# Performance work log

Measured on AMD Instinct MI355X. Metric: run time of the kernel, lower is better.

The kernel has to match this reference:

```python
import jax, jax.numpy as jnp
import numpy as np

N = 5000        # nodes
F = 7699        # node feature dim (fixed by code)
E = 40000       # edges
ED = 3          # edge_dim (fixed by code)
H1, C1 = 4, 1024
H2, C2 = 1, 1024
NUM_OUT = 128
NEG_SLOPE = 0.2


def _glorot(key, shape):
    fan_in = shape[0]
    return jax.random.normal(key, shape, jnp.float32) / np.float32(np.sqrt(fan_in))


def setup_inputs() -> dict:
    key = jax.random.key(0)
    ks = jax.random.split(key, 16)
    x = jax.random.normal(ks[0], (N, F), jnp.float32)
    src = jax.random.randint(ks[1], (E,), 0, N)
    dst = jax.random.randint(ks[2], (E,), 0, N)
    src = jnp.where(src == dst, (src + 1) % N, src)  # no pre-existing self loops
    edge_index = jnp.stack([src, dst]).astype(jnp.int32)
    edge_attr = jax.random.normal(ks[3], (E, ED), jnp.float32)
    inp = {
        "x": x, "edge_index": edge_index, "edge_attr": edge_attr,
        # GATv2Conv #1: 7699 -> 1024, heads=4, edge_dim=3
        "W1l": _glorot(ks[4], (F, H1 * C1)), "b1l": jnp.zeros((H1 * C1,), jnp.float32),
        "W1r": _glorot(ks[5], (F, H1 * C1)), "b1r": jnp.zeros((H1 * C1,), jnp.float32),
        "W1e": _glorot(ks[6], (ED, H1 * C1)),
        "att1": _glorot(ks[7], (H1, C1)),
        "bias1": jnp.zeros((H1 * C1,), jnp.float32),
        # GATv2Conv #2: 4096 -> 1024, heads=1, edge_dim=3
        "W2l": _glorot(ks[8], (H1 * C1, H2 * C2)), "b2l": jnp.zeros((H2 * C2,), jnp.float32),
        "W2r": _glorot(ks[9], (H1 * C1, H2 * C2)), "b2r": jnp.zeros((H2 * C2,), jnp.float32),
        "W2e": _glorot(ks[10], (ED, H2 * C2)),
        "att2": _glorot(ks[11], (H2, C2)),
        "bias2": jnp.zeros((H2 * C2,), jnp.float32),
        # final Linear(1024, num_outputs)
        "Wlin": _glorot(ks[12], (C2, NUM_OUT)), "blin": jnp.zeros((NUM_OUT,), jnp.float32),
    }
    return inp


def gatv2_layer(x, src, dst, edge_attr, Wl, bl, Wr, br, We, att, bias, heads, out_ch):
    """PyG GATv2Conv with add_self_loops=True, fill_value='mean', concat=True."""
    n = x.shape[0]
    # self-loop edge_attr = mean of incoming edge attrs per node (fill_value='mean')
    deg = jax.ops.segment_sum(jnp.ones((src.shape[0],), jnp.float32), dst, num_segments=n)
    loop_attr = jax.ops.segment_sum(edge_attr, dst, num_segments=n) / jnp.maximum(deg, 1.0)[:, None]
    idx = jnp.arange(n, dtype=src.dtype)
    srcf = jnp.concatenate([src, idx])
    dstf = jnp.concatenate([dst, idx])
    ea = jnp.concatenate([edge_attr, loop_attr], axis=0)
    xl = (x @ Wl + bl).reshape(n, heads, out_ch)   # lin_l (source)
    xr = (x @ Wr + br).reshape(n, heads, out_ch)   # lin_r (target)
    ee = (ea @ We).reshape(-1, heads, out_ch)       # lin_edge (no bias)
    e = jax.nn.leaky_relu(xl[srcf] + xr[dstf] + ee, NEG_SLOPE)  # [E', H, C]
    logit = jnp.einsum('ehc,hc->eh', e, att)                     # [E', H]
    # segment softmax over destination nodes (every node has a self loop)
    m = jax.lax.stop_gradient(jax.ops.segment_max(logit, dstf, num_segments=n))
    a = jnp.exp(logit - m[dstf])
    denom = jax.ops.segment_sum(a, dstf, num_segments=n)
    alpha = a / (denom[dstf] + 1e-16)
    out = jax.ops.segment_sum(alpha[:, :, None] * xl[srcf], dstf, num_segments=n)  # [N,H,C]
    return out.reshape(n, heads * out_ch) + bias


def reference(x, edge_index, edge_attr,
              W1l, b1l, W1r, b1r, W1e, att1, bias1,
              W2l, b2l, W2r, b2r, W2e, att2, bias2,
              Wlin, blin):
    src, dst = edge_index[0], edge_index[1]
    h = gatv2_layer(x, src, dst, edge_attr, W1l, b1l, W1r, b1r, W1e, att1, bias1, H1, C1)
    h = gatv2_layer(h, src, dst, edge_attr, W2l, b2l, W2r, b2r, W2e, att2, bias2, H2, C2)
    return h @ Wlin + blin
```

## Files before the change

kernel.cpp:

```cpp
#include <hip/hip_runtime.h>
#include <cstdint>
#include <cstddef>

#define N_NODES 5000
#define F_IN    7699
#define KP1     7712
#define KT1     241
#define MP      5120
#define E_EDGES 40000
#define EFULL   45000
#define HC1     4096
#define N1      8192
#define HC2     1024
#define N2      2048
#define NOUT    128
#define GM      (MP / 256)

typedef __bf16 bf16x8 __attribute__((ext_vector_type(8)));
typedef float  f32x4  __attribute__((ext_vector_type(4)));
typedef float  f32x16 __attribute__((ext_vector_type(16)));
typedef unsigned short u16x8 __attribute__((ext_vector_type(8)));
typedef _Float16 f16;
typedef _Float16 f16x8 __attribute__((ext_vector_type(8)));

using as1_uchar = unsigned char __attribute__((address_space(1)));
using as3_uchar = unsigned char __attribute__((address_space(3)));

__device__ __forceinline__ unsigned short f2bf(float f) {
  union { float f; unsigned int u; } v; v.f = f;
  return (unsigned short)((v.u + 0x7fffu + ((v.u >> 16) & 1u)) >> 16);
}
__device__ __forceinline__ float bf2f(unsigned short h) {
  union { unsigned int u; float f; } v; v.u = ((unsigned int)h) << 16;
  return v.f;
}

__device__ __forceinline__ void gload16(const void* g, void* l) {
  __builtin_amdgcn_global_load_lds(
      reinterpret_cast<const as1_uchar*>(reinterpret_cast<uintptr_t>(g)),
      reinterpret_cast<as3_uchar*>(reinterpret_cast<uintptr_t>(l)),
      16, 0, 0);
}



__global__ void k_split_x(const float* __restrict__ x, unsigned short* __restrict__ hi,
                          unsigned short* __restrict__ lo) {
  const int C8 = KP1 / 8;
  int ci = blockIdx.x * 256 + threadIdx.x;
  if (ci >= MP * C8) return;
  int r = ci / C8, c8 = ci % C8;
  int c = c8 * 8;
  u16x8 hb, lb;
  #pragma unroll
  for (int j = 0; j < 8; ++j) {
    float v = 0.f;
    if (r < N_NODES && (c + j) < F_IN) v = x[(size_t)r * F_IN + c + j];
    unsigned short h = f2bf(v);
    hb[j] = h; lb[j] = f2bf(v - bf2f(h));
  }
  size_t off = ((size_t)((r >> 7) * KT1 + (c >> 5)) * 4 + ((c >> 3) & 3)) * 1024 + (r & 127) * 8;
  *(u16x8*)&hi[off] = hb;
  *(u16x8*)&lo[off] = lb;
}


__global__ void k_split_w(const float* __restrict__ W,
                          unsigned short* __restrict__ hi, unsigned short* __restrict__ lo,
                          int K, int Nsrc, int c0, int KT, int rowOffset) {
  __shared__ float tile[32][33];
  const int tid = threadIdx.x;
  const int kt = blockIdx.x;
  const int n0 = blockIdx.y * 32;
  #pragma unroll
  for (int i = tid >> 5; i < 32; i += 8) {
    int k = kt * 32 + i;
    tile[i][tid & 31] = (k < K) ? W[(size_t)k * Nsrc + c0 + n0 + (tid & 31)] : 0.f;
  }
  __syncthreads();
  if (tid < 128) {
    const int nn = tid >> 2, kc = (tid & 3) << 3;
    const int n = rowOffset + n0 + nn;
    u16x8 hb, lb;
    #pragma unroll
    for (int j = 0; j < 8; ++j) {
      float v = tile[kc + j][nn];
      unsigned short h = f2bf(v);
      hb[j] = h; lb[j] = f2bf(v - bf2f(h));
    }
    size_t off = ((size_t)((n >> 7) * KT + kt) * 4 + (kc >> 3)) * 1024 + (n & 127) * 8;
    *(u16x8*)&hi[off] = hb;
    *(u16x8*)&lo[off] = lb;
  }
}


template <int OF16>
__global__ __launch_bounds__(256, 1) void k_gemm_bb(
    const unsigned short* __restrict__ Ahi, const unsigned short* __restrict__ Alo,
    const unsigned short* __restrict__ Bhi, const unsigned short* __restrict__ Blo,
    void* __restrict__ Cp, const float* __restrict__ bias0, const float* __restrict__ bias1,
    int halfN, int M, int Nc, int ldC, int KT32, int nbn)
{
  __shared__ __align__(16) unsigned short S[3 * 16384];

  const int tid = threadIdx.x;
  const int lane = tid & 63;
  const int w = tid >> 6;
  const int wm = w >> 1, wn = w & 1;

  const int nwg = gridDim.x;
  const int qq = nwg >> 3, rr = nwg & 7;
  const int xcd = blockIdx.x & 7, idx = blockIdx.x >> 3;
  const int wg = (xcd < rr ? xcd * (qq + 1) : rr * (qq + 1) + (xcd - rr) * qq) + idx;
  const int bm = wg / nbn, bn = wg % nbn;

  f32x16 acc[4][4] = {};

  const unsigned short* gbase = (w == 0) ? Ahi : (w == 1) ? Alo : (w == 2) ? Bhi : Blo;
  const int brow = (w < 2) ? bm * 2 : bn * 2;
  const unsigned short* gsrc[8];
  int dd[8];
  #pragma unroll
  for (int d = 0; d < 8; ++d) {
    const int t = d >> 2, p = (d >> 1) & 1, hf = d & 1;
    gsrc[d] = gbase + (size_t)(brow + t) * KT32 * 4096 + p * 1024 + hf * 512 + lane * 8;
    dd[d] = w * 4096 + t * 2048 + p * 1024 + hf * 512;
  }

  auto stage = [&](int kt16, int bufo) {
    const size_t o = (size_t)kt16 * 2048;
    #pragma unroll
    for (int d = 0; d < 8; ++d) gload16(gsrc[d] + o, &S[bufo + dd[d]]);
  };

  const int r5 = lane & 31, h5 = lane >> 5;
  int ra[4], cb[4];
  #pragma unroll
  for (int i = 0; i < 4; ++i) ra[i] = wm * 2048 + h5 * 1024 + (i * 32 + r5) * 8;
  #pragma unroll
  for (int j = 0; j < 4; ++j) cb[j] = 8192 + wn * 2048 + h5 * 1024 + (j * 32 + r5) * 8;

  const int KT16 = KT32 * 2;

  stage(0, 0);
  stage(1, 16384);
  asm volatile("s_waitcnt vmcnt(8)" ::: "memory");
  __builtin_amdgcn_s_barrier();

  int ocur = 0, onxt = 16384, onx2 = 32768;
  for (int kt = 0; kt < KT16; ++kt) {
    const int ks = (kt + 2 < KT16) ? kt + 2 : KT16 - 1;
    stage(ks, onx2);

    bf16x8 ah[4], al[4], bh[4], bl[4];
    #pragma unroll
    for (int i = 0; i < 4; ++i) {
      ah[i] = *(const bf16x8*)&S[ocur + ra[i]];
      al[i] = *(const bf16x8*)&S[ocur + 4096 + ra[i]];
    }
    #pragma unroll
    for (int j = 0; j < 4; ++j) {
      bh[j] = *(const bf16x8*)&S[ocur + cb[j]];
      bl[j] = *(const bf16x8*)&S[ocur + 4096 + cb[j]];
    }

    __builtin_amdgcn_s_setprio(1);
    #pragma unroll
    for (int j = 0; j < 4; ++j)
      #pragma unroll
      for (int i = 0; i < 4; ++i) {
        acc[i][j] = __builtin_amdgcn_mfma_f32_32x32x16_bf16(ah[i], bh[j], acc[i][j], 0, 0, 0);
        acc[i][j] = __builtin_amdgcn_mfma_f32_32x32x16_bf16(al[i], bh[j], acc[i][j], 0, 0, 0);
        acc[i][j] = __builtin_amdgcn_mfma_f32_32x32x16_bf16(ah[i], bl[j], acc[i][j], 0, 0, 0);
      }
    __builtin_amdgcn_s_setprio(0);

    asm volatile("s_waitcnt vmcnt(8)" ::: "memory");
    __builtin_amdgcn_s_barrier();
    const int t = ocur; ocur = onxt; onxt = onx2; onx2 = t;
  }

  #pragma unroll
  for (int i = 0; i < 4; ++i) {
    #pragma unroll
    for (int j = 0; j < 4; ++j) {
      const int gc = bn * 256 + wn * 128 + j * 32 + r5;
      if (gc < Nc) {
        const float bv = (gc < halfN) ? bias0[gc] : bias1[gc - halfN];
        #pragma unroll
        for (int reg = 0; reg < 16; ++reg) {
          const int gr = bm * 256 + wm * 128 + i * 32 + (reg & 3) + 8 * (reg >> 2) + 4 * h5;
          if (gr < M) {
            float v = acc[i][j][reg] + bv;
            if (OF16) ((f16*)Cp)[(size_t)gr * ldC + gc] = (f16)v;
            else      ((float*)Cp)[(size_t)gr * ldC + gc] = v;
          }
        }
      }
    }
  }
}


__global__ void k_deg(const int* __restrict__ dst, const float* __restrict__ ea,
                      float* __restrict__ deg, float* __restrict__ lattr, int E) {
  int e = blockIdx.x * 256 + threadIdx.x;
  if (e >= E) return;
  int d = dst[e];
  atomicAdd(&deg[d], 1.f);
  atomicAdd(&lattr[d * 3 + 0], ea[e * 3 + 0]);
  atomicAdd(&lattr[d * 3 + 1], ea[e * 3 + 1]);
  atomicAdd(&lattr[d * 3 + 2], ea[e * 3 + 2]);
}

__global__ void k_lattr_fin(float* __restrict__ lattr, const float* __restrict__ deg, int n) {
  int i = blockIdx.x * 256 + threadIdx.x;
  if (i >= n) return;
  float dv = fmaxf(deg[i], 1.f);
  lattr[i * 3 + 0] /= dv; lattr[i * 3 + 1] /= dv; lattr[i * 3 + 2] /= dv;
}

__global__ void k_eafull(const float* __restrict__ ea, const float* __restrict__ lattr,
                         float* __restrict__ eaf, int E, int n) {
  int e = blockIdx.x * 256 + threadIdx.x;
  if (e >= E + n) return;
  const float* s = (e < E) ? &ea[(size_t)e * 3] : &lattr[(size_t)(e - E) * 3];
  eaf[e * 3 + 0] = s[0]; eaf[e * 3 + 1] = s[1]; eaf[e * 3 + 2] = s[2];
}

__global__ void k_count(const int* __restrict__ dst, int* __restrict__ cnt, int E, int n) {
  int e = blockIdx.x * 256 + threadIdx.x;
  if (e >= E + n) return;
  int d = (e < E) ? dst[e] : (e - E);
  atomicAdd(&cnt[d], 1);
}

__global__ void k_scan(const int* __restrict__ cnt, int* __restrict__ rowptr, int n) {
  int lane = threadIdx.x;
  int run = 0;
  for (int base = 0; base < n; base += 64) {
    int i = base + lane;
    int v = (i < n) ? cnt[i] : 0;
    #pragma unroll
    for (int off = 1; off < 64; off <<= 1) {
      int t = __shfl_up(v, off, 64);
      if (lane >= off) v += t;
    }
    if (i < n) rowptr[i + 1] = run + v;
    run += __shfl(v, 63, 64);
  }
  if (lane == 0) rowptr[0] = 0;
}

__global__ void k_fill(const int* __restrict__ dst, const int* __restrict__ rowptr,
                       int* __restrict__ fillc, int* __restrict__ elist, int E, int n) {
  int e = blockIdx.x * 256 + threadIdx.x;
  if (e >= E + n) return;
  int d = (e < E) ? dst[e] : (e - E);
  int pos = rowptr[d] + atomicAdd(&fillc[d], 1);
  elist[pos] = e;
}


template <int H, int ITERS>
__global__ __launch_bounds__(256) void k_logit(
    const f16* __restrict__ xl, const f16* __restrict__ xr, int strideX,
    const float* __restrict__ eaf, const float* __restrict__ We, const float* __restrict__ att,
    const int* __restrict__ src, const int* __restrict__ dst, int E,
    float* __restrict__ logit)
{
  const int e = blockIdx.x;
  const int tid = threadIdx.x;
  int s, d;
  if (e < E) { s = src[e]; d = dst[e]; } else { s = e - E; d = s; }
  const float ea0 = eaf[e * 3 + 0], ea1 = eaf[e * 3 + 1], ea2 = eaf[e * 3 + 2];
  constexpr int HC = ITERS * 256;
  const f16* rl = xl + (size_t)s * strideX;
  const f16* rr = xr + (size_t)d * strideX;
  float acc[H];
  #pragma unroll
  for (int h = 0; h < H; ++h) acc[h] = 0.f;
  #pragma unroll
  for (int i = 0; i < ITERS; ++i) {
    int hc = tid + (i << 8);
    float v = (float)rl[hc] + (float)rr[hc]
            + ea0 * We[hc] + ea1 * We[HC + hc] + ea2 * We[2 * HC + hc];
    v = (v > 0.f) ? v : 0.2f * v;
    acc[i >> 2] += v * att[hc];
  }
  __shared__ float red[H][4];
  const int lane = tid & 63, wv = tid >> 6;
  #pragma unroll
  for (int h = 0; h < H; ++h) {
    float v = acc[h];
    #pragma unroll
    for (int off = 32; off > 0; off >>= 1) v += __shfl_down(v, off, 64);
    if (lane == 0) red[h][wv] = v;
  }
  __syncthreads();
  if (tid < H)
    logit[(size_t)e * H + tid] = red[tid][0] + red[tid][1] + red[tid][2] + red[tid][3];
}

template <int H>
__global__ void k_stats(const float* __restrict__ logit, const int* __restrict__ rowptr,
                        const int* __restrict__ elist, float* __restrict__ mb, float* __restrict__ db)
{
  const int n = blockIdx.x;
  const int lane = threadIdx.x;
  const int start = rowptr[n], end = rowptr[n + 1];
  #pragma unroll
  for (int h = 0; h < H; ++h) {
    float m = -1e30f;
    for (int p = start + lane; p < end; p += 64)
      m = fmaxf(m, logit[(size_t)elist[p] * H + h]);
    #pragma unroll
    for (int off = 32; off > 0; off >>= 1) m = fmaxf(m, __shfl_down(m, off, 64));
    m = __shfl(m, 0, 64);
    float sum = 0.f;
    for (int p = start + lane; p < end; p += 64)
      sum += __expf(logit[(size_t)elist[p] * H + h] - m);
    #pragma unroll
    for (int off = 32; off > 0; off >>= 1) sum += __shfl_down(sum, off, 64);
    if (lane == 0) { mb[n * H + h] = m; db[n * H + h] = sum; }
  }
}

template <int H, int NC8, int KTo>
__global__ __launch_bounds__(256) void k_agg(
    const f16* __restrict__ xl, int strideX,
    const int* __restrict__ rowptr, const int* __restrict__ elist, const int* __restrict__ src,
    const float* __restrict__ logit, const float* __restrict__ mb, const float* __restrict__ db,
    const float* __restrict__ bias,
    unsigned short* __restrict__ ohi, unsigned short* __restrict__ olo, int E)
{
  const int n = blockIdx.x;
  const int tid = threadIdx.x;
  constexpr int HC = H * 1024;
  float acc[NC8][8];
  #pragma unroll
  for (int q = 0; q < NC8; ++q)
    #pragma unroll
    for (int j = 0; j < 8; ++j) acc[q][j] = 0.f;
  const int start = rowptr[n], end = rowptr[n + 1];
  float mloc[H], dloc[H];
  #pragma unroll
  for (int h = 0; h < H; ++h) { mloc[h] = mb[n * H + h]; dloc[h] = db[n * H + h] + 1e-16f; }
  for (int p = start; p < end; ++p) {
    const int e = elist[p];
    const int s = (e < E) ? src[e] : (e - E);
    float al[H];
    #pragma unroll
    for (int h = 0; h < H; ++h)
      al[h] = __expf(logit[(size_t)e * H + h] - mloc[h]) / dloc[h];
    const f16* row = xl + (size_t)s * strideX;
    #pragma unroll
    for (int q = 0; q < NC8; ++q) {
      const int c8 = tid + q * 256;
      if (c8 * 8 < HC) {
        float a = (H == 4) ? ((tid & 128) ? al[2 * q + 1] : al[2 * q]) : al[0];
        f16x8 v = *(const f16x8*)(row + c8 * 8);
        #pragma unroll
        for (int j = 0; j < 8; ++j) acc[q][j] += a * (float)v[j];
      }
    }
  }
  #pragma unroll
  for (int q = 0; q < NC8; ++q) {
    const int c8 = tid + q * 256;
    if (c8 * 8 < HC) {
      u16x8 hb, lb;
      #pragma unroll
      for (int j = 0; j < 8; ++j) {
        float v = acc[q][j] + bias[c8 * 8 + j];
        unsigned short h = f2bf(v);
        hb[j] = h; lb[j] = f2bf(v - bf2f(h));
      }
      size_t off = ((size_t)((n >> 7) * KTo + (c8 >> 2)) * 4 + (c8 & 3)) * 1024 + (n & 127) * 8;
      *(u16x8*)&ohi[off] = hb;
      *(u16x8*)&olo[off] = lb;
    }
  }
}


extern "C" void kernel_launch(void* const* d_in, const int* in_sizes, int n_in,
                              void* d_out, int out_size, void* d_ws, size_t ws_size,
                              hipStream_t stream) {
  const float* x    = (const float*)d_in[0];
  const int*   eidx = (const int*)d_in[1];
  const float* eattr= (const float*)d_in[2];
  const float* W1l  = (const float*)d_in[3];
  const float* b1l  = (const float*)d_in[4];
  const float* W1r  = (const float*)d_in[5];
  const float* b1r  = (const float*)d_in[6];
  const float* W1e  = (const float*)d_in[7];
  const float* att1 = (const float*)d_in[8];
  const float* bias1= (const float*)d_in[9];
  const float* W2l  = (const float*)d_in[10];
  const float* b2l  = (const float*)d_in[11];
  const float* W2r  = (const float*)d_in[12];
  const float* b2r  = (const float*)d_in[13];
  const float* W2e  = (const float*)d_in[14];
  const float* att2 = (const float*)d_in[15];
  const float* bias2= (const float*)d_in[16];
  const float* Wlin = (const float*)d_in[17];
  const float* blin = (const float*)d_in[18];
  float* out = (float*)d_out;

  char* ws = (char*)d_ws;
  const int* srcp = eidx;
  const int* dstp = eidx + E_EDGES;

  auto alignup = [](size_t v) { return (v + 255) & ~(size_t)255; };

  size_t mo = 0;
  auto take = [&](size_t sz) { size_t r = mo; mo = alignup(mo + sz); return r; };
  const size_t oLATTR = take((size_t)N_NODES * 3 * 4);
  const size_t oDEG   = take((size_t)N_NODES * 4);
  const size_t oEAF   = take((size_t)EFULL * 3 * 4);
  const size_t oCNT   = take((size_t)N_NODES * 4);
  const size_t oROW   = take((size_t)(N_NODES + 1) * 4);
  const size_t oFILL  = take((size_t)N_NODES * 4);
  const size_t oELIST = take((size_t)EFULL * 4);
  const size_t oLOGIT = take((size_t)EFULL * 4 * 4);
  const size_t oMB    = take((size_t)N_NODES * 4 * 4);
  const size_t oDB    = take((size_t)N_NODES * 4 * 4);
  const size_t oXHI   = take((size_t)MP * KP1 * 2);
  const size_t oXLO   = take((size_t)MP * KP1 * 2);
  const size_t oXLR   = take((size_t)N_NODES * N1 * 2);
  const size_t oBH    = take((size_t)N1 * KP1 * 2);
  const size_t oBL    = take((size_t)N1 * KP1 * 2);
  if (ws_size < mo) return;

  const size_t oH1HI = oXHI;
  const size_t oH1LO = oXLO;
  const size_t oXLR2 = oXLR;
  const size_t oH2HI = oXLR + 32ull * 1024 * 1024;
  const size_t oH2LO = oXLR + 48ull * 1024 * 1024;
  const size_t oB2H  = oBH;
  const size_t oB2L  = oBH + 32ull * 1024 * 1024;
  const size_t oB3H  = oBH;
  const size_t oB3L  = oBH + 1ull * 1024 * 1024;

  unsigned short* XHI  = (unsigned short*)(ws + oXHI);
  unsigned short* XLO  = (unsigned short*)(ws + oXLO);
  f16*            XLR  = (f16*)(ws + oXLR);
  unsigned short* BH   = (unsigned short*)(ws + oBH);
  unsigned short* BL   = (unsigned short*)(ws + oBL);
  float*          LATTR= (float*)(ws + oLATTR);
  float*          DEG  = (float*)(ws + oDEG);
  float*          EAF  = (float*)(ws + oEAF);
  int*            CNT  = (int*)(ws + oCNT);
  int*            ROWP = (int*)(ws + oROW);
  int*            FILLC= (int*)(ws + oFILL);
  int*            ELIST= (int*)(ws + oELIST);
  float*          LOGIT= (float*)(ws + oLOGIT);
  float*          MB   = (float*)(ws + oMB);
  float*          DB   = (float*)(ws + oDB);
  unsigned short* H1HI = (unsigned short*)(ws + oH1HI);
  unsigned short* H1LO = (unsigned short*)(ws + oH1LO);
  f16*            XLR2 = (f16*)(ws + oXLR2);
  unsigned short* H2HI = (unsigned short*)(ws + oH2HI);
  unsigned short* H2LO = (unsigned short*)(ws + oH2LO);
  unsigned short* B2H  = (unsigned short*)(ws + oB2H);
  unsigned short* B2L  = (unsigned short*)(ws + oB2L);
  unsigned short* B3H  = (unsigned short*)(ws + oB3H);
  unsigned short* B3L  = (unsigned short*)(ws + oB3L);

  hipMemsetAsync(ws + oDEG,   0, (size_t)N_NODES * 4, stream);
  hipMemsetAsync(ws + oLATTR, 0, (size_t)N_NODES * 3 * 4, stream);
  hipMemsetAsync(ws + oCNT,   0, (size_t)N_NODES * 4, stream);
  hipMemsetAsync(ws + oFILL,  0, (size_t)N_NODES * 4, stream);

  const int gE  = (E_EDGES + 255) / 256;
  const int gEF = (EFULL + 255) / 256;
  const int gN  = (N_NODES + 255) / 256;

  k_deg<<<gE, 256, 0, stream>>>(dstp, eattr, DEG, LATTR, E_EDGES);
  k_lattr_fin<<<gN, 256, 0, stream>>>(LATTR, DEG, N_NODES);
  k_eafull<<<gEF, 256, 0, stream>>>(eattr, LATTR, EAF, E_EDGES, N_NODES);
  k_count<<<gEF, 256, 0, stream>>>(dstp, CNT, E_EDGES, N_NODES);
  k_scan<<<1, 64, 0, stream>>>(CNT, ROWP, N_NODES);
  k_fill<<<gEF, 256, 0, stream>>>(dstp, ROWP, FILLC, ELIST, E_EDGES, N_NODES);

  k_split_x<<<MP * (KP1 / 8) / 256, 256, 0, stream>>>(x, XHI, XLO);
  k_split_w<<<dim3(KT1, HC1 / 32), 256, 0, stream>>>(W1l, BH, BL, F_IN, HC1, 0, KT1, 0);
  k_split_w<<<dim3(KT1, HC1 / 32), 256, 0, stream>>>(W1r, BH, BL, F_IN, HC1, 0, KT1, HC1);
  k_gemm_bb<1><<<GM * (N1 / 256), 256, 0, stream>>>(
      XHI, XLO, BH, BL, XLR, b1l, b1r, HC1, N_NODES, N1, N1, KT1, N1 / 256);

  k_logit<4, 16><<<EFULL, 256, 0, stream>>>(XLR, XLR + HC1, N1, EAF, W1e, att1, srcp, dstp, E_EDGES, LOGIT);
  k_stats<4><<<N_NODES, 64, 0, stream>>>(LOGIT, ROWP, ELIST, MB, DB);
  hipMemsetAsync(ws + oH1HI, 0, (size_t)MP * HC1 * 2, stream);
  hipMemsetAsync(ws + oH1LO, 0, (size_t)MP * HC1 * 2, stream);
  k_agg<4, 2, HC1 / 32><<<N_NODES, 256, 0, stream>>>(
      XLR, N1, ROWP, ELIST, srcp, LOGIT, MB, DB, bias1, H1HI, H1LO, E_EDGES);

  k_split_w<<<dim3(HC1 / 32, HC2 / 32), 256, 0, stream>>>(W2l, B2H, B2L, HC1, HC2, 0, HC1 / 32, 0);
  k_split_w<<<dim3(HC1 / 32, HC2 / 32), 256, 0, stream>>>(W2r, B2H, B2L, HC1, HC2, 0, HC1 / 32, HC2);
  k_gemm_bb<1><<<GM * (N2 / 256), 256, 0, stream>>>(
      H1HI, H1LO, B2H, B2L, XLR2, b2l, b2r, HC2, N_NODES, N2, N2, HC1 / 32, N2 / 256);

  k_logit<1, 4><<<EFULL, 256, 0, stream>>>(XLR2, XLR2 + HC2, N2, EAF, W2e, att2, srcp, dstp, E_EDGES, LOGIT);
  k_stats<1><<<N_NODES, 64, 0, stream>>>(LOGIT, ROWP, ELIST, MB, DB);
  hipMemsetAsync(ws + oH2HI, 0, (size_t)MP * HC2 * 2, stream);
  hipMemsetAsync(ws + oH2LO, 0, (size_t)MP * HC2 * 2, stream);
  k_agg<1, 1, HC2 / 32><<<N_NODES, 256, 0, stream>>>(
      XLR2, N2, ROWP, ELIST, srcp, LOGIT, MB, DB, bias2, H2HI, H2LO, E_EDGES);

  hipMemsetAsync(ws + oB3H, 0, (size_t)2 * 32 * 4096 * 2, stream);
  hipMemsetAsync(ws + oB3L, 0, (size_t)2 * 32 * 4096 * 2, stream);
  k_split_w<<<dim3(HC2 / 32, NOUT / 32), 256, 0, stream>>>(Wlin, B3H, B3L, HC2, NOUT, 0, HC2 / 32, 0);
  k_gemm_bb<0><<<GM * 1, 256, 0, stream>>>(
      H2HI, H2LO, B3H, B3L, out, blin, blin, NOUT, N_NODES, NOUT, NOUT, HC2 / 32, 1);
}
```

Before: 3.003 ms.

## Retile split-bf16 GEMM to 256x128 with 8 waves and 4-stage LDS ring

The GEMM now uses a 256x128 output tile with 512 threads (8 waves, each computing 64x64), instead of a 256x256 tile with 4 waves. The LDS pipeline becomes a four-buffer ring that prefetches three K-steps ahead. The loop is unrolled by two and double-buffers register fragments, so LDS reads for the next step overlap the MFMAs of the current one. The aim is higher occupancy and better latency hiding. In exchange, B-tile reuse per block drops, global traffic for A rises, and the loop assumes an even number of K-steps.

```diff
diff --git a/kernel.cpp b/kernel.cpp
--- a/kernel.cpp
+++ b/kernel.cpp
@@ -96,13 +96,13 @@
 
 
 template <int OF16>
-__global__ __launch_bounds__(256, 1) void k_gemm_bb(
+__global__ __launch_bounds__(512, 2) void k_gemm_bb(
     const unsigned short* __restrict__ Ahi, const unsigned short* __restrict__ Alo,
     const unsigned short* __restrict__ Bhi, const unsigned short* __restrict__ Blo,
     void* __restrict__ Cp, const float* __restrict__ bias0, const float* __restrict__ bias1,
     int halfN, int M, int Nc, int ldC, int KT32, int nbn)
 {
-  __shared__ __align__(16) unsigned short S[3 * 16384];
+  __shared__ __align__(16) unsigned short S[4 * 12288];
 
   const int tid = threadIdx.x;
   const int lane = tid & 63;
@@ -115,82 +115,103 @@
   const int wg = (xcd < rr ? xcd * (qq + 1) : rr * (qq + 1) + (xcd - rr) * qq) + idx;
   const int bm = wg / nbn, bn = wg % nbn;
 
-  f32x16 acc[4][4] = {};
-
-  const unsigned short* gbase = (w == 0) ? Ahi : (w == 1) ? Alo : (w == 2) ? Bhi : Blo;
-  const int brow = (w < 2) ? bm * 2 : bn * 2;
-  const unsigned short* gsrc[8];
-  int dd[8];
-  #pragma unroll
-  for (int d = 0; d < 8; ++d) {
-    const int t = d >> 2, p = (d >> 1) & 1, hf = d & 1;
-    gsrc[d] = gbase + (size_t)(brow + t) * KT32 * 4096 + p * 1024 + hf * 512 + lane * 8;
-    dd[d] = w * 4096 + t * 2048 + p * 1024 + hf * 512;
+  f32x16 acc[2][2] = {};
+
+  const unsigned short* gsrc[3];
+  int dd[3];
+  #pragma unroll
+  for (int s = 0; s < 3; ++s) {
+    const int q = w * 3 + s;
+    const unsigned short* base; int dOff; size_t rowoff; int p, hf;
+    if (q < 8)       { int r_ = q;      base = Ahi; int t = r_ >> 2; p = (r_ >> 1) & 1; hf = r_ & 1;
+                       dOff = t * 2048 + p * 1024 + hf * 512; rowoff = (size_t)(bm * 2 + t) * KT32 * 4096; }
+    else if (q < 16) { int r_ = q - 8;  base = Alo; int t = r_ >> 2; p = (r_ >> 1) & 1; hf = r_ & 1;
+                       dOff = 4096 + t * 2048 + p * 1024 + hf * 512; rowoff = (size_t)(bm * 2 + t) * KT32 * 4096; }
+    else if (q < 20) { int r_ = q - 16; base = Bhi; p = (r_ >> 1) & 1; hf = r_ & 1;
+                       dOff = 8192 + p * 1024 + hf * 512; rowoff = (size_t)bn * KT32 * 4096; }
+    else             { int r_ = q - 20; base = Blo; p = (r_ >> 1) & 1; hf = r_ & 1;
+                       dOff = 10240 + p * 1024 + hf * 512; rowoff = (size_t)bn * KT32 * 4096; }
+    gsrc[s] = base + rowoff + p * 1024 + hf * 512 + lane * 8;
+    dd[s] = dOff;
   }
 
   auto stage = [&](int kt16, int bufo) {
     const size_t o = (size_t)kt16 * 2048;
     #pragma unroll
-    for (int d = 0; d < 8; ++d) gload16(gsrc[d] + o, &S[bufo + dd[d]]);
+    for (int s = 0; s < 3; ++s) gload16(gsrc[s] + o, &S[bufo + dd[s]]);
   };
 
   const int r5 = lane & 31, h5 = lane >> 5;
-  int ra[4], cb[4];
-  #pragma unroll
-  for (int i = 0; i < 4; ++i) ra[i] = wm * 2048 + h5 * 1024 + (i * 32 + r5) * 8;
-  #pragma unroll
-  for (int j = 0; j < 4; ++j) cb[j] = 8192 + wn * 2048 + h5 * 1024 + (j * 32 + r5) * 8;
-
-  const int KT16 = KT32 * 2;
-
-  stage(0, 0);
-  stage(1, 16384);
-  asm volatile("s_waitcnt vmcnt(8)" ::: "memory");
-  __builtin_amdgcn_s_barrier();
-
-  int ocur = 0, onxt = 16384, onx2 = 32768;
-  for (int kt = 0; kt < KT16; ++kt) {
-    const int ks = (kt + 2 < KT16) ? kt + 2 : KT16 - 1;
-    stage(ks, onx2);
-
-    bf16x8 ah[4], al[4], bh[4], bl[4];
-    #pragma unroll
-    for (int i = 0; i < 4; ++i) {
-      ah[i] = *(const bf16x8*)&S[ocur + ra[i]];
-      al[i] = *(const bf16x8*)&S[ocur + 4096 + ra[i]];
-    }
-    #pragma unroll
-    for (int j = 0; j < 4; ++j) {
-      bh[j] = *(const bf16x8*)&S[ocur + cb[j]];
-      bl[j] = *(const bf16x8*)&S[ocur + 4096 + cb[j]];
-    }
-
+  const int tA = wm >> 1;
+  const int rrA = (wm & 1) * 64;
+  int ra[2], cb[2];
+  #pragma unroll
+  for (int i = 0; i < 2; ++i) ra[i] = tA * 2048 + h5 * 1024 + (rrA + i * 32 + r5) * 8;
+  #pragma unroll
+  for (int j = 0; j < 2; ++j) cb[j] = 8192 + h5 * 1024 + (wn * 64 + j * 32 + r5) * 8;
+
+  struct Frags { bf16x8 ah[2], al[2], bh[2], bl[2]; };
+  auto rdfr = [&](Frags& f, int bufo) {
+    #pragma unroll
+    for (int i = 0; i < 2; ++i) {
+      f.ah[i] = *(const bf16x8*)&S[bufo + ra[i]];
+      f.al[i] = *(const bf16x8*)&S[bufo + 4096 + ra[i]];
+    }
+    #pragma unroll
+    for (int j = 0; j < 2; ++j) {
+      f.bh[j] = *(const bf16x8*)&S[bufo + cb[j]];
+      f.bl[j] = *(const bf16x8*)&S[bufo + 2048 + cb[j]];
+    }
+  };
+  auto domfma = [&](Frags& f) {
     __builtin_amdgcn_s_setprio(1);
     #pragma unroll
-    for (int j = 0; j < 4; ++j)
+    for (int j = 0; j < 2; ++j)
       #pragma unroll
-      for (int i = 0; i < 4; ++i) {
-        acc[i][j] = __builtin_amdgcn_mfma_f32_32x32x16_bf16(ah[i], bh[j], acc[i][j], 0, 0, 0);
-        acc[i][j] = __builtin_amdgcn_mfma_f32_32x32x16_bf16(al[i], bh[j], acc[i][j], 0, 0, 0);
-        acc[i][j] = __builtin_amdgcn_mfma_f32_32x32x16_bf16(ah[i], bl[j], acc[i][j], 0, 0, 0);
+      for (int i = 0; i < 2; ++i) {
+        acc[i][j] = __builtin_amdgcn_mfma_f32_32x32x16_bf16(f.ah[i], f.bh[j], acc[i][j], 0, 0, 0);
+        acc[i][j] = __builtin_amdgcn_mfma_f32_32x32x16_bf16(f.al[i], f.bh[j], acc[i][j], 0, 0, 0);
+        acc[i][j] = __builtin_amdgcn_mfma_f32_32x32x16_bf16(f.ah[i], f.bl[j], acc[i][j], 0, 0, 0);
       }
     __builtin_amdgcn_s_setprio(0);
-
-    asm volatile("s_waitcnt vmcnt(8)" ::: "memory");
+  };
+
+  const int KT16 = KT32 * 2;
+
+  stage(0, 0);
+  stage(1, 12288);
+  stage(2, 24576);
+  asm volatile("s_waitcnt vmcnt(3)" ::: "memory");
+  __builtin_amdgcn_s_barrier();
+  Frags fA, fB;
+  rdfr(fA, 0);
+
+  int o0 = 0, o1 = 12288, o2 = 24576, o3 = 36864;
+  for (int kt = 0; kt < KT16; kt += 2) {
+    stage((kt + 3 < KT16) ? kt + 3 : KT16 - 1, o3);
+    rdfr(fB, o1);
+    domfma(fA);
+    asm volatile("s_waitcnt vmcnt(3)" ::: "memory");
     __builtin_amdgcn_s_barrier();
-    const int t = ocur; ocur = onxt; onxt = onx2; onx2 = t;
-  }
-
-  #pragma unroll
-  for (int i = 0; i < 4; ++i) {
-    #pragma unroll
-    for (int j = 0; j < 4; ++j) {
-      const int gc = bn * 256 + wn * 128 + j * 32 + r5;
+    stage((kt + 4 < KT16) ? kt + 4 : KT16 - 1, o0);
+    rdfr(fA, o2);
+    domfma(fB);
+    asm volatile("s_waitcnt vmcnt(3)" ::: "memory");
+    __builtin_amdgcn_s_barrier();
+    int t0 = o0, t1 = o1;
+    o0 = o2; o1 = o3; o2 = t0; o3 = t1;
+  }
+
+  #pragma unroll
+  for (int i = 0; i < 2; ++i) {
+    #pragma unroll
+    for (int j = 0; j < 2; ++j) {
+      const int gc = bn * 128 + wn * 64 + j * 32 + r5;
       if (gc < Nc) {
         const float bv = (gc < halfN) ? bias0[gc] : bias1[gc - halfN];
         #pragma unroll
         for (int reg = 0; reg < 16; ++reg) {
-          const int gr = bm * 256 + wm * 128 + i * 32 + (reg & 3) + 8 * (reg >> 2) + 4 * h5;
+          const int gr = bm * 256 + wm * 64 + i * 32 + (reg & 3) + 8 * (reg >> 2) + 4 * h5;
           if (gr < M) {
             float v = acc[i][j][reg] + bv;
             if (OF16) ((f16*)Cp)[(size_t)gr * ldC + gc] = (f16)v;
@@ -488,8 +509,8 @@
   k_split_x<<<MP * (KP1 / 8) / 256, 256, 0, stream>>>(x, XHI, XLO);
   k_split_w<<<dim3(KT1, HC1 / 32), 256, 0, stream>>>(W1l, BH, BL, F_IN, HC1, 0, KT1, 0);
   k_split_w<<<dim3(KT1, HC1 / 32), 256, 0, stream>>>(W1r, BH, BL, F_IN, HC1, 0, KT1, HC1);
-  k_gemm_bb<1><<<GM * (N1 / 256), 256, 0, stream>>>(
-      XHI, XLO, BH, BL, XLR, b1l, b1r, HC1, N_NODES, N1, N1, KT1, N1 / 256);
+  k_gemm_bb<1><<<GM * (N1 / 128), 512, 0, stream>>>(
+      XHI, XLO, BH, BL, XLR, b1l, b1r, HC1, N_NODES, N1, N1, KT1, N1 / 128);
 
   k_logit<4, 16><<<EFULL, 256, 0, stream>>>(XLR, XLR + HC1, N1, EAF, W1e, att1, srcp, dstp, E_EDGES, LOGIT);
   k_stats<4><<<N_NODES, 64, 0, stream>>>(LOGIT, ROWP, ELIST, MB, DB);
@@ -500,8 +521,8 @@
 
   k_split_w<<<dim3(HC1 / 32, HC2 / 32), 256, 0, stream>>>(W2l, B2H, B2L, HC1, HC2, 0, HC1 / 32, 0);
   k_split_w<<<dim3(HC1 / 32, HC2 / 32), 256, 0, stream>>>(W2r, B2H, B2L, HC1, HC2, 0, HC1 / 32, HC2);
-  k_gemm_bb<1><<<GM * (N2 / 256), 256, 0, stream>>>(
-      H1HI, H1LO, B2H, B2L, XLR2, b2l, b2r, HC2, N_NODES, N2, N2, HC1 / 32, N2 / 256);
+  k_gemm_bb<1><<<GM * (N2 / 128), 512, 0, stream>>>(
+      H1HI, H1LO, B2H, B2L, XLR2, b2l, b2r, HC2, N_NODES, N2, N2, HC1 / 32, N2 / 128);
 
   k_logit<1, 4><<<EFULL, 256, 0, stream>>>(XLR2, XLR2 + HC2, N2, EAF, W2e, att2, srcp, dstp, E_EDGES, LOGIT);
   k_stats<1><<<N_NODES, 64, 0, stream>>>(LOGIT, ROWP, ELIST, MB, DB);
@@ -510,9 +531,9 @@
   k_agg<1, 1, HC2 / 32><<<N_NODES, 256, 0, stream>>>(
       XLR2, N2, ROWP, ELIST, srcp, LOGIT, MB, DB, bias2, H2HI, H2LO, E_EDGES);
 
-  hipMemsetAsync(ws + oB3H, 0, (size_t)2 * 32 * 4096 * 2, stream);
-  hipMemsetAsync(ws + oB3L, 0, (size_t)2 * 32 * 4096 * 2, stream);
+  hipMemsetAsync(ws + oB3H, 0, (size_t)32 * 4096 * 2, stream);
+  hipMemsetAsync(ws + oB3L, 0, (size_t)32 * 4096 * 2, stream);
   k_split_w<<<dim3(HC2 / 32, NOUT / 32), 256, 0, stream>>>(Wlin, B3H, B3L, HC2, NOUT, 0, HC2 / 32, 0);
-  k_gemm_bb<0><<<GM * 1, 256, 0, stream>>>(
+  k_gemm_bb<0><<<GM * 1, 512, 0, stream>>>(
       H2HI, H2LO, B3H, B3L, out, blin, blin, NOUT, N_NODES, NOUT, NOUT, HC2 / 32, 1);
 }
```

Result: faster. 2.802 ms (-6.7%).
